# Performance work log

Hardware: AMD Instinct MI355X
Metric: run time of the kernel (lower is better)

The kernel has to match this reference:

```python
import jax, jax.numpy as jnp
import numpy as np
from jax import lax

TEMPERATURE = 30.0
BN_EPS = 1e-5


def setup_inputs() -> dict:
    key = jax.random.key(0)
    ks = jax.random.split(key, 9)
    B, H, W, C_in = 32, 64, 64, 128
    n_filters, r_filters, n_kernels = 128, 4, 4
    x = jax.random.normal(ks[0], (B, H, W, C_in), dtype=jnp.float32)
    reduction_kernel = jax.random.normal(ks[1], (C_in, r_filters), dtype=jnp.float32) * 0.02
    attention_kernel = jax.random.normal(ks[2], (r_filters, n_kernels), dtype=jnp.float32) * 0.02
    conv_kernels = jax.random.normal(ks[3], (n_kernels, 3, 3, C_in, n_filters), dtype=jnp.float32) * 0.05
    bias = jax.random.normal(ks[4], (n_kernels, n_filters), dtype=jnp.float32) * 0.05
    bn_scale = jax.random.uniform(ks[5], (n_filters,), dtype=jnp.float32, minval=0.5, maxval=1.5)
    bn_bias = jax.random.normal(ks[6], (n_filters,), dtype=jnp.float32) * 0.1
    bn_mean = jax.random.normal(ks[7], (n_filters,), dtype=jnp.float32) * 0.1
    bn_var = jax.random.uniform(ks[8], (n_filters,), dtype=jnp.float32, minval=0.5, maxval=1.5)
    return {"x": x, "reduction_kernel": reduction_kernel, "attention_kernel": attention_kernel,
            "conv_kernels": conv_kernels, "bias": bias, "bn_scale": bn_scale, "bn_bias": bn_bias,
            "bn_mean": bn_mean, "bn_var": bn_var}


def reference(x, reduction_kernel, attention_kernel, conv_kernels, bias, bn_scale, bn_bias, bn_mean, bn_var):
    # x: [B,H,W,C_in] NHWC. Inference mode (training=False): BN uses running stats.
    B = x.shape[0]
    # Squeeze-style routing: global average pool -> reduce -> relu -> attention over experts.
    pool = jnp.mean(x, axis=(1, 2))                             # [B, C_in]
    pool_red = jax.nn.relu(pool @ reduction_kernel)             # [B, r]
    attention = jax.nn.softmax((pool_red @ attention_kernel) / TEMPERATURE, axis=-1)  # [B, K]
    # Soft mixture of conv expert kernels, per sample.
    w_mixed = jnp.einsum('bk,khwio->bhwio', attention, conv_kernels)  # [B,kH,kW,C_in,F]

    def per_sample_conv(xi, wi):
        # xi: [H,W,C_in], wi: [kH,kW,C_in,F]
        return lax.conv_general_dilated(xi[None], wi, window_strides=(1, 1), padding='SAME',
                                        dimension_numbers=('NHWC', 'HWIO', 'NHWC'))[0]

    y = jax.vmap(per_sample_conv)(x, w_mixed)                   # [B,H,W,F]
    b_mixed = attention @ bias                                  # [B, F]
    y = y + b_mixed[:, None, None, :]
    # BatchNorm (inference) + relu
    inv = bn_scale * lax.rsqrt(bn_var + BN_EPS)
    y = (y - bn_mean) * inv + bn_bias
    return jax.nn.relu(y)
```

## Files before the change

### kernel.cpp

```cpp
#include <hip/hip_runtime.h>

typedef short bf16x8 __attribute__((ext_vector_type(8)));
typedef float f32x4 __attribute__((ext_vector_type(4)));
typedef unsigned int u32x4 __attribute__((ext_vector_type(4)));
typedef unsigned short u16x4 __attribute__((ext_vector_type(4)));

__device__ __forceinline__ unsigned short f2bf(float f) {
  unsigned u = __builtin_bit_cast(unsigned, f);
  u = (u + 0x7FFFu + ((u >> 16) & 1u)) >> 16;
  return (unsigned short)u;
}

__global__ __launch_bounds__(256) void k_pool_cvt(const float* __restrict__ x,
                                                  unsigned short* __restrict__ xb,
                                                  float* __restrict__ pp) {
  const int slice = blockIdx.x;
  const int b = blockIdx.y;
  const int t = threadIdx.x;
  const int c4 = (t & 31) * 4;
  const int seg = t >> 5;
  const size_t base = ((size_t)b * 4096 + slice * 256 + seg * 32) * 128;
  const float* xp = x + base;
  unsigned short* xbp = xb + base;
  f32x4 s = {0.f, 0.f, 0.f, 0.f};
  for (int p = 0; p < 32; ++p) {
    f32x4 v = *(const f32x4*)(xp + p * 128 + c4);
    s += v;
    u16x4 h;
    h.x = f2bf(v.x); h.y = f2bf(v.y); h.z = f2bf(v.z); h.w = f2bf(v.w);
    *(u16x4*)(xbp + p * 128 + c4) = h;
  }
  __shared__ f32x4 red[256];
  red[t] = s;
  __syncthreads();
  if (t < 32) {
    f32x4 tot = red[t];
#pragma unroll
    for (int g = 1; g < 8; ++g) tot += red[g * 32 + t];
    *(f32x4*)(pp + (size_t)(b * 16 + slice) * 128 + t * 4) = tot;
  }
}

__global__ __launch_bounds__(128) void k_route(const float* __restrict__ pp,
    const float* __restrict__ redk, const float* __restrict__ attk,
    const float* __restrict__ bias, const float* __restrict__ bns,
    const float* __restrict__ bnb, const float* __restrict__ bnm,
    const float* __restrict__ bnv,
    float* __restrict__ att_ws, float* __restrict__ beta_ws,
    float* __restrict__ alpha_ws) {
  const int b = blockIdx.x, t = threadIdx.x;
  __shared__ float pool[128];
  __shared__ float att[4];
  {
    float s = 0.f;
    for (int i = 0; i < 16; ++i) s += pp[(size_t)(b * 16 + i) * 128 + t];
    pool[t] = s * (1.f / 4096.f);
  }
  __syncthreads();
  if (t == 0) {
    float pr[4];
    for (int r = 0; r < 4; ++r) {
      float s = 0.f;
      for (int c = 0; c < 128; ++c) s += pool[c] * redk[c * 4 + r];
      pr[r] = fmaxf(s, 0.f);
    }
    float lgt[4]; float mx = -1e30f;
    for (int k = 0; k < 4; ++k) {
      float s = 0.f;
      for (int r = 0; r < 4; ++r) s += pr[r] * attk[r * 4 + k];
      lgt[k] = s * (1.f / 30.f);
      mx = fmaxf(mx, lgt[k]);
    }
    float den = 0.f;
    for (int k = 0; k < 4; ++k) { lgt[k] = expf(lgt[k] - mx); den += lgt[k]; }
    for (int k = 0; k < 4; ++k) { att[k] = lgt[k] / den; att_ws[b * 4 + k] = att[k]; }
  }
  __syncthreads();
  {
    float bm = 0.f;
    for (int k = 0; k < 4; ++k) bm += att[k] * bias[k * 128 + t];
    const float inv = bns[t] * rsqrtf(bnv[t] + 1e-5f);
    beta_ws[b * 128 + t] = (bm - bnm[t]) * inv + bnb[t];
    alpha_ws[t] = inv;
  }
}

__global__ __launch_bounds__(256) void k_mixw(const float* __restrict__ ck,
                                              const float* __restrict__ att_ws,
                                              unsigned short* __restrict__ w_ws) {
  const int tap = blockIdx.x;
  const int b = blockIdx.y;
  const int t = threadIdx.x;
  const float a0 = att_ws[b * 4 + 0], a1 = att_ws[b * 4 + 1];
  const float a2 = att_ws[b * 4 + 2], a3 = att_ws[b * 4 + 3];
  const float* ckp = ck + (size_t)tap * 16384;
  __shared__ unsigned short lds_t[128 * 136];
#pragma unroll 4
  for (int it = 0; it < 16; ++it) {
    const int i4 = t + it * 256;
    const int idx = i4 * 4;
    const int c = idx >> 7, f = idx & 127;
    f32x4 v0 = *(const f32x4*)(ckp + idx);
    f32x4 v1 = *(const f32x4*)(ckp + idx + 147456);
    f32x4 v2 = *(const f32x4*)(ckp + idx + 2 * 147456);
    f32x4 v3 = *(const f32x4*)(ckp + idx + 3 * 147456);
#pragma unroll
    for (int e = 0; e < 4; ++e)
      lds_t[(f + e) * 136 + c] = f2bf(a0 * v0[e] + a1 * v1[e] + a2 * v2[e] + a3 * v3[e]);
  }
  __syncthreads();
#pragma unroll
  for (int it = 0; it < 8; ++it) {
    const int m = t + it * 256;
    const int f = m >> 4, oo = m & 15;
    const int h = oo >> 3, o = oo & 7;
    unsigned short* dst = w_ws + ((size_t)b * 18 + h * 9 + tap) * 8192
                        + (size_t)(f * 8 + (o ^ (f & 7))) * 8;
    *(bf16x8*)dst = *(const bf16x8*)(lds_t + f * 136 + oo * 8);
  }
}

__device__ __forceinline__ void stage_w16(char* dst, const unsigned short* src, int t) {
#pragma unroll
  for (int j = 0; j < 2; ++j) {
    const int i = t + j * 512;
    __builtin_amdgcn_global_load_lds(
        (const __attribute__((address_space(1))) void*)(src + (size_t)i * 8),
        (__attribute__((address_space(3))) void*)(dst + i * 16), 16, 0, 0);
  }
}

__device__ __forceinline__ void stage_x_half(char* xt, const unsigned short* xbp,
                                             int r0, int h, int t) {
  const int pix = t >> 3;
  const int oct = (t & 7) ^ ((t >> 3) & 7);
#pragma unroll
  for (int j = 0; j < 6; ++j) {
    const int rr = r0 - 1 + j;
    char* dst = xt + j * 8192 + t * 16;
    if ((unsigned)rr < 64u) {
      __builtin_amdgcn_global_load_lds(
          (const __attribute__((address_space(1))) void*)
              (xbp + ((size_t)(rr * 64 + pix)) * 128 + h * 64 + oct * 8),
          (__attribute__((address_space(3))) void*)dst, 16, 0, 0);
    } else {
      *(u32x4*)dst = (u32x4){0, 0, 0, 0};
    }
  }
}

__global__ __launch_bounds__(512, 4) void k_conv(const unsigned short* __restrict__ xb,
                                                 const unsigned short* __restrict__ w_ws,
                                                 const float* __restrict__ alpha_ws,
                                                 const float* __restrict__ beta_ws,
                                                 float* __restrict__ out) {
  extern __shared__ char lds[];
  char* xt = lds;
  char* wlds = lds + 49152;

  const int orig = blockIdx.x;
  const int wg = (orig & 7) * 64 + (orig >> 3);
  const int b = wg >> 4;
  const int tile = wg & 15;
  const int t = threadIdx.x;
  const int lane = t & 63, wid = t >> 6;
  const int wm = wid >> 1, wn = wid & 1;
  const int lr = lane & 15, lg = lane >> 4;
  const int r0 = tile * 4;

  const unsigned short* xbp = xb + (size_t)b * 4096 * 128;
  const unsigned short* wsrc = w_ws + (size_t)b * 18 * 8192;

  f32x4 acc[4][4] = {};
  const bf16x8 zero = {};

  stage_x_half(xt, xbp, r0, 0, t);
  stage_w16(wlds, wsrc, t);
  asm volatile("s_waitcnt vmcnt(0) lgkmcnt(0)" ::: "memory");
  __builtin_amdgcn_s_barrier();
  asm volatile("" ::: "memory");

  for (int s = 0; s < 18; ++s) {
    const int tap = s % 9;
    char* cb = wlds + ((s & 1) << 14);
    if (s == 9) stage_x_half(xt, xbp, r0, 1, t);
    if (s < 17) stage_w16(wlds + (((s + 1) & 1) << 14),
                          wsrc + (size_t)(s + 1) * 8192, t);
    if (s == 9)       asm volatile("s_waitcnt vmcnt(2) lgkmcnt(0)" ::: "memory");
    else if (s < 17)  asm volatile("s_waitcnt vmcnt(2)" ::: "memory");
    else              asm volatile("s_waitcnt vmcnt(0)" ::: "memory");
    __builtin_amdgcn_s_barrier();
    asm volatile("" ::: "memory");

    const int dh = tap / 3 - 1, dw = tap % 3 - 1;
    const int jrow = wm + dh + 1;
#pragma unroll
    for (int kc = 0; kc < 2; ++kc) {
      bf16x8 afr[4], bfr[4];
#pragma unroll
      for (int mf = 0; mf < 4; ++mf) {
        const int col = mf * 16 + lr + dw;
        const int a = ((jrow * 64 + col) * 128 + kc * 64 + lg * 16) ^ ((col & 7) << 4);
        afr[mf] = ((unsigned)col < 64u) ? *(const bf16x8*)(xt + a) : zero;
      }
#pragma unroll
      for (int nf = 0; nf < 4; ++nf) {
        const int f = wn * 64 + nf * 16 + lr;
        const int a = (f * 128 + kc * 64 + lg * 16) ^ ((f & 7) << 4);
        bfr[nf] = *(const bf16x8*)(cb + a);
      }
      __builtin_amdgcn_s_setprio(1);
#pragma unroll
      for (int mf = 0; mf < 4; ++mf)
#pragma unroll
        for (int nf = 0; nf < 4; ++nf)
          acc[mf][nf] = __builtin_amdgcn_mfma_f32_16x16x32_bf16(afr[mf], bfr[nf],
                                                                acc[mf][nf], 0, 0, 0);
      __builtin_amdgcn_s_setprio(0);
    }
    asm volatile("" ::: "memory");
    __builtin_amdgcn_s_barrier();
  }

  float af[4], bt[4];
#pragma unroll
  for (int nf = 0; nf < 4; ++nf) {
    const int f = wn * 64 + nf * 16 + lr;
    af[nf] = alpha_ws[f];
    bt[nf] = beta_ws[b * 128 + f];
  }
  float* op = out + (size_t)b * 4096 * 128;
  const int row = r0 + wm;
#pragma unroll
  for (int mf = 0; mf < 4; ++mf) {
#pragma unroll
    for (int r = 0; r < 4; ++r) {
      const int col = mf * 16 + lg * 4 + r;
#pragma unroll
      for (int nf = 0; nf < 4; ++nf) {
        const int f = wn * 64 + nf * 16 + lr;
        const float v = acc[mf][nf][r] * af[nf] + bt[nf];
        op[(size_t)(row * 64 + col) * 128 + f] = fmaxf(v, 0.f);
      }
    }
  }
}

extern "C" void kernel_launch(void* const* d_in, const int* in_sizes, int n_in,
                              void* d_out, int out_size, void* d_ws, size_t ws_size,
                              hipStream_t stream) {
  const float* x    = (const float*)d_in[0];
  const float* redk = (const float*)d_in[1];
  const float* attk = (const float*)d_in[2];
  const float* ck   = (const float*)d_in[3];
  const float* bias = (const float*)d_in[4];
  const float* bns  = (const float*)d_in[5];
  const float* bnbb = (const float*)d_in[6];
  const float* bnm  = (const float*)d_in[7];
  const float* bnv  = (const float*)d_in[8];
  float* out = (float*)d_out;

  char* ws = (char*)d_ws;
  unsigned short* xb   = (unsigned short*)ws;
  unsigned short* w_ws = (unsigned short*)(ws + 33554432);
  float* pp       = (float*)(ws + 42991616);
  float* att_ws   = (float*)(ws + 43253760);
  float* beta_ws  = (float*)(ws + 43254272);
  float* alpha_ws = (float*)(ws + 43270656);

  k_pool_cvt<<<dim3(16, 32), 256, 0, stream>>>(x, xb, pp);
  k_route<<<32, 128, 0, stream>>>(pp, redk, attk, bias, bns, bnbb, bnm, bnv,
                                  att_ws, beta_ws, alpha_ws);
  k_mixw<<<dim3(9, 32), 256, 0, stream>>>(ck, att_ws, w_ws);
  k_conv<<<512, 512, 81920, stream>>>(xb, w_ws, alpha_ws, beta_ws, out);
}
```

Before: 83.03 us.

## Halve conv block to 4 waves, each computing all 128 filters per row

The conv kernel moves from 512 threads (8 waves, 4x2 wave grid) to 256 threads (4 waves), with each wave now covering a full 64-pixel row across all 128 filters. That gives 4x8 MFMA tiles per wave, so each A fragment is reused across twice as many B fragments. Staging loops are adjusted for the smaller thread count, and the wait counts change to match. LDS addresses and boundary masks are precomputed outside the tap loop, and the loop is fully unrolled to cut address arithmetic. The cost is much higher register pressure from 128 accumulators per lane and fewer waves per block to hide latency.

```diff
diff --git a/kernel.cpp b/kernel.cpp
--- a/kernel.cpp
+++ b/kernel.cpp
@@ -122,8 +122,8 @@
 
 __device__ __forceinline__ void stage_w16(char* dst, const unsigned short* src, int t) {
 #pragma unroll
-  for (int j = 0; j < 2; ++j) {
-    const int i = t + j * 512;
+  for (int j = 0; j < 4; ++j) {
+    const int i = t + j * 256;
     __builtin_amdgcn_global_load_lds(
         (const __attribute__((address_space(1))) void*)(src + (size_t)i * 8),
         (__attribute__((address_space(3))) void*)(dst + i * 16), 16, 0, 0);
@@ -132,16 +132,19 @@
 
 __device__ __forceinline__ void stage_x_half(char* xt, const unsigned short* xbp,
                                              int r0, int h, int t) {
-  const int pix = t >> 3;
-  const int oct = (t & 7) ^ ((t >> 3) & 7);
-#pragma unroll
-  for (int j = 0; j < 6; ++j) {
-    const int rr = r0 - 1 + j;
-    char* dst = xt + j * 8192 + t * 16;
+#pragma unroll
+  for (int j = 0; j < 12; ++j) {
+    const int i = t + j * 256;
+    const int jr = i >> 9;
+    const int pix = (i & 511) >> 3;
+    const int oct = i & 7;
+    const int soct = oct ^ (pix & 7);
+    const int rr = r0 - 1 + jr;
+    char* dst = xt + i * 16;
     if ((unsigned)rr < 64u) {
       __builtin_amdgcn_global_load_lds(
           (const __attribute__((address_space(1))) void*)
-              (xbp + ((size_t)(rr * 64 + pix)) * 128 + h * 64 + oct * 8),
+              (xbp + ((size_t)(rr * 64 + pix)) * 128 + h * 64 + soct * 8),
           (__attribute__((address_space(3))) void*)dst, 16, 0, 0);
     } else {
       *(u32x4*)dst = (u32x4){0, 0, 0, 0};
@@ -149,7 +152,7 @@
   }
 }
 
-__global__ __launch_bounds__(512, 4) void k_conv(const unsigned short* __restrict__ xb,
+__global__ __launch_bounds__(256, 2) void k_conv(const unsigned short* __restrict__ xb,
                                                  const unsigned short* __restrict__ w_ws,
                                                  const float* __restrict__ alpha_ws,
                                                  const float* __restrict__ beta_ws,
@@ -163,16 +166,33 @@
   const int b = wg >> 4;
   const int tile = wg & 15;
   const int t = threadIdx.x;
-  const int lane = t & 63, wid = t >> 6;
-  const int wm = wid >> 1, wn = wid & 1;
+  const int lane = t & 63, wm = t >> 6;
   const int lr = lane & 15, lg = lane >> 4;
   const int r0 = tile * 4;
 
   const unsigned short* xbp = xb + (size_t)b * 4096 * 128;
   const unsigned short* wsrc = w_ws + (size_t)b * 18 * 8192;
 
-  f32x4 acc[4][4] = {};
+  f32x4 acc[4][8] = {};
   const bf16x8 zero = {};
+
+  int abase[3][4];
+  bool aval[3][4];
+#pragma unroll
+  for (int d = 0; d < 3; ++d)
+#pragma unroll
+    for (int mf = 0; mf < 4; ++mf) {
+      const int col = mf * 16 + lr + d - 1;
+      const bool v = (unsigned)col < 64u;
+      aval[d][mf] = v;
+      abase[d][mf] = v ? ((col * 128 + lg * 16) ^ ((col & 7) << 4)) : 0;
+    }
+  int bbase[8];
+#pragma unroll
+  for (int nf = 0; nf < 8; ++nf) {
+    const int f = nf * 16 + lr;
+    bbase[nf] = (f * 128 + lg * 16) ^ ((f & 7) << 4);
+  }
 
   stage_x_half(xt, xbp, r0, 0, t);
   stage_w16(wlds, wsrc, t);
@@ -180,40 +200,38 @@
   __builtin_amdgcn_s_barrier();
   asm volatile("" ::: "memory");
 
+#pragma unroll
   for (int s = 0; s < 18; ++s) {
     const int tap = s % 9;
     char* cb = wlds + ((s & 1) << 14);
     if (s == 9) stage_x_half(xt, xbp, r0, 1, t);
     if (s < 17) stage_w16(wlds + (((s + 1) & 1) << 14),
                           wsrc + (size_t)(s + 1) * 8192, t);
-    if (s == 9)       asm volatile("s_waitcnt vmcnt(2) lgkmcnt(0)" ::: "memory");
-    else if (s < 17)  asm volatile("s_waitcnt vmcnt(2)" ::: "memory");
+    if (s == 9)       asm volatile("s_waitcnt vmcnt(4) lgkmcnt(0)" ::: "memory");
+    else if (s < 17)  asm volatile("s_waitcnt vmcnt(4)" ::: "memory");
     else              asm volatile("s_waitcnt vmcnt(0)" ::: "memory");
     __builtin_amdgcn_s_barrier();
     asm volatile("" ::: "memory");
 
-    const int dh = tap / 3 - 1, dw = tap % 3 - 1;
-    const int jrow = wm + dh + 1;
+    const int d = tap % 3;
+    const int jrow = wm + tap / 3;
 #pragma unroll
     for (int kc = 0; kc < 2; ++kc) {
-      bf16x8 afr[4], bfr[4];
+      const int kx = kc << 6;
+      bf16x8 afr[4], bfr[8];
 #pragma unroll
       for (int mf = 0; mf < 4; ++mf) {
-        const int col = mf * 16 + lr + dw;
-        const int a = ((jrow * 64 + col) * 128 + kc * 64 + lg * 16) ^ ((col & 7) << 4);
-        afr[mf] = ((unsigned)col < 64u) ? *(const bf16x8*)(xt + a) : zero;
+        bf16x8 v = *(const bf16x8*)(xt + ((abase[d][mf] ^ kx) + jrow * 8192));
+        afr[mf] = aval[d][mf] ? v : zero;
       }
 #pragma unroll
-      for (int nf = 0; nf < 4; ++nf) {
-        const int f = wn * 64 + nf * 16 + lr;
-        const int a = (f * 128 + kc * 64 + lg * 16) ^ ((f & 7) << 4);
-        bfr[nf] = *(const bf16x8*)(cb + a);
-      }
+      for (int nf = 0; nf < 8; ++nf)
+        bfr[nf] = *(const bf16x8*)(cb + (bbase[nf] ^ kx));
       __builtin_amdgcn_s_setprio(1);
 #pragma unroll
       for (int mf = 0; mf < 4; ++mf)
 #pragma unroll
-        for (int nf = 0; nf < 4; ++nf)
+        for (int nf = 0; nf < 8; ++nf)
           acc[mf][nf] = __builtin_amdgcn_mfma_f32_16x16x32_bf16(afr[mf], bfr[nf],
                                                                 acc[mf][nf], 0, 0, 0);
       __builtin_amdgcn_s_setprio(0);
@@ -222,10 +240,10 @@
     __builtin_amdgcn_s_barrier();
   }
 
-  float af[4], bt[4];
-#pragma unroll
-  for (int nf = 0; nf < 4; ++nf) {
-    const int f = wn * 64 + nf * 16 + lr;
+  float af[8], bt[8];
+#pragma unroll
+  for (int nf = 0; nf < 8; ++nf) {
+    const int f = nf * 16 + lr;
     af[nf] = alpha_ws[f];
     bt[nf] = beta_ws[b * 128 + f];
   }
@@ -237,8 +255,8 @@
     for (int r = 0; r < 4; ++r) {
       const int col = mf * 16 + lg * 4 + r;
 #pragma unroll
-      for (int nf = 0; nf < 4; ++nf) {
-        const int f = wn * 64 + nf * 16 + lr;
+      for (int nf = 0; nf < 8; ++nf) {
+        const int f = nf * 16 + lr;
         const float v = acc[mf][nf][r] * af[nf] + bt[nf];
         op[(size_t)(row * 64 + col) * 128 + f] = fmaxf(v, 0.f);
       }
@@ -272,5 +290,5 @@
   k_route<<<32, 128, 0, stream>>>(pp, redk, attk, bias, bns, bnbb, bnm, bnv,
                                   att_ws, beta_ws, alpha_ws);
   k_mixw<<<dim3(9, 32), 256, 0, stream>>>(ck, att_ws, w_ws);
-  k_conv<<<512, 512, 81920, stream>>>(xb, w_ws, alpha_ws, beta_ws, out);
-}
+  k_conv<<<512, 256, 81920, stream>>>(xb, w_ws, alpha_ws, beta_ws, out);
+}
```

Measured after the change: 89.35 us. 1.08x slower.

## Restructure expert-weight mixing to reuse loaded slices across batches; simplify conv barriers

Applied to the files above, without the earlier changes.

k_mixw now launches 144 blocks, one per (tap, C_in quarter, F quarter). Each block loads one slice of all four expert kernels once into LDS and writes the mixed bf16 weights for all 32 samples. Before, each of the 288 blocks re-read the full tap weights per sample. In k_conv, the stage-then-barrier-then-compute order becomes compute-then-wait-then-barrier with a single barrier per step, and the second x half is staged after step 8. The loop now waits for all outstanding loads before each barrier, which may expose load latency that vmcnt(2) used to hide.

```diff
diff --git a/kernel.cpp b/kernel.cpp
--- a/kernel.cpp
+++ b/kernel.cpp
@@ -88,35 +88,47 @@
 __global__ __launch_bounds__(256) void k_mixw(const float* __restrict__ ck,
                                               const float* __restrict__ att_ws,
                                               unsigned short* __restrict__ w_ws) {
-  const int tap = blockIdx.x;
-  const int b = blockIdx.y;
+  const int bx = blockIdx.x;
+  const int tap = bx >> 4;
+  const int cq = (bx >> 2) & 3;
+  const int fq = bx & 3;
   const int t = threadIdx.x;
-  const float a0 = att_ws[b * 4 + 0], a1 = att_ws[b * 4 + 1];
-  const float a2 = att_ws[b * 4 + 2], a3 = att_ws[b * 4 + 3];
-  const float* ckp = ck + (size_t)tap * 16384;
-  __shared__ unsigned short lds_t[128 * 136];
-#pragma unroll 4
-  for (int it = 0; it < 16; ++it) {
-    const int i4 = t + it * 256;
-    const int idx = i4 * 4;
-    const int c = idx >> 7, f = idx & 127;
-    f32x4 v0 = *(const f32x4*)(ckp + idx);
-    f32x4 v1 = *(const f32x4*)(ckp + idx + 147456);
-    f32x4 v2 = *(const f32x4*)(ckp + idx + 2 * 147456);
-    f32x4 v3 = *(const f32x4*)(ckp + idx + 3 * 147456);
-#pragma unroll
-    for (int e = 0; e < 4; ++e)
-      lds_t[(f + e) * 136 + c] = f2bf(a0 * v0[e] + a1 * v1[e] + a2 * v2[e] + a3 * v3[e]);
-  }
-  __syncthreads();
-#pragma unroll
-  for (int it = 0; it < 8; ++it) {
-    const int m = t + it * 256;
-    const int f = m >> 4, oo = m & 15;
-    const int h = oo >> 3, o = oo & 7;
-    unsigned short* dst = w_ws + ((size_t)b * 18 + h * 9 + tap) * 8192
-                        + (size_t)(f * 8 + (o ^ (f & 7))) * 8;
-    *(bf16x8*)dst = *(const bf16x8*)(lds_t + f * 136 + oo * 8);
+  __shared__ float cw[4][32][32];
+  __shared__ float attl[128];
+  if (t < 128) attl[t] = att_ws[t];
+  {
+    const int k = t >> 6, c = (t & 63) >> 1, f0 = (t & 1) * 16;
+    const float* src = ck + ((size_t)(k * 9 + tap) * 128 + cq * 32 + c) * 128
+                          + fq * 32 + f0;
+    *(f32x4*)&cw[k][c][f0]      = *(const f32x4*)(src);
+    *(f32x4*)&cw[k][c][f0 + 4]  = *(const f32x4*)(src + 4);
+    *(f32x4*)&cw[k][c][f0 + 8]  = *(const f32x4*)(src + 8);
+    *(f32x4*)&cw[k][c][f0 + 12] = *(const f32x4*)(src + 12);
+  }
+  __syncthreads();
+  const int f = t & 31, o = (t >> 5) & 3, sh = t >> 7;
+  const int fp = fq * 32 + f;
+  const int h = cq >> 1;
+  const int oslab = (cq & 1) * 4 + o;
+  const int chunk = fp * 8 + (oslab ^ (fp & 7));
+  float wv[4][8];
+#pragma unroll
+  for (int k = 0; k < 4; ++k)
+#pragma unroll
+    for (int j = 0; j < 8; ++j) wv[k][j] = cw[k][o * 8 + j][f];
+#pragma unroll
+  for (int bs = 0; bs < 16; ++bs) {
+    const int b = sh * 16 + bs;
+    const float a0 = attl[b * 4 + 0], a1 = attl[b * 4 + 1];
+    const float a2 = attl[b * 4 + 2], a3 = attl[b * 4 + 3];
+    bf16x8 ov;
+#pragma unroll
+    for (int j = 0; j < 8; ++j) {
+      const float v = a0 * wv[0][j] + a1 * wv[1][j] + a2 * wv[2][j] + a3 * wv[3][j];
+      ov[j] = (short)f2bf(v);
+    }
+    *(bf16x8*)(w_ws + (size_t)b * 147456 + (size_t)(h * 9 + tap) * 8192
+               + (size_t)chunk * 8) = ov;
   }
 }
 
@@ -183,14 +195,8 @@
   for (int s = 0; s < 18; ++s) {
     const int tap = s % 9;
     char* cb = wlds + ((s & 1) << 14);
-    if (s == 9) stage_x_half(xt, xbp, r0, 1, t);
     if (s < 17) stage_w16(wlds + (((s + 1) & 1) << 14),
                           wsrc + (size_t)(s + 1) * 8192, t);
-    if (s == 9)       asm volatile("s_waitcnt vmcnt(2) lgkmcnt(0)" ::: "memory");
-    else if (s < 17)  asm volatile("s_waitcnt vmcnt(2)" ::: "memory");
-    else              asm volatile("s_waitcnt vmcnt(0)" ::: "memory");
-    __builtin_amdgcn_s_barrier();
-    asm volatile("" ::: "memory");
 
     const int dh = tap / 3 - 1, dw = tap % 3 - 1;
     const int jrow = wm + dh + 1;
@@ -219,7 +225,18 @@
       __builtin_amdgcn_s_setprio(0);
     }
     asm volatile("" ::: "memory");
-    __builtin_amdgcn_s_barrier();
+
+    if (s == 8) {
+      __builtin_amdgcn_s_barrier();
+      stage_x_half(xt, xbp, r0, 1, t);
+      asm volatile("s_waitcnt vmcnt(0) lgkmcnt(0)" ::: "memory");
+      __builtin_amdgcn_s_barrier();
+      asm volatile("" ::: "memory");
+    } else if (s < 17) {
+      asm volatile("s_waitcnt vmcnt(0)" ::: "memory");
+      __builtin_amdgcn_s_barrier();
+      asm volatile("" ::: "memory");
+    }
   }
 
   float af[4], bt[4];
@@ -271,6 +288,6 @@
   k_pool_cvt<<<dim3(16, 32), 256, 0, stream>>>(x, xb, pp);
   k_route<<<32, 128, 0, stream>>>(pp, redk, attk, bias, bns, bnbb, bnm, bnv,
                                   att_ws, beta_ws, alpha_ws);
-  k_mixw<<<dim3(9, 32), 256, 0, stream>>>(ck, att_ws, w_ws);
+  k_mixw<<<144, 256, 0, stream>>>(ck, att_ws, w_ws);
   k_conv<<<512, 512, 81920, stream>>>(xb, w_ws, alpha_ws, beta_ws, out);
 }
```

Result: faster. 75.41 us (median of 2 runs) (-9.2%).
